# Kernel tuning notes

Measured on AMD Instinct MI355X. Metric: run time of the kernel, lower is better.

## Reference

```python
import jax, jax.numpy as jnp
import numpy as np

N_NODES = 50000


def gcn_layer(x, src, dst, W, b):
    # GCNConv: out = D^{-1/2} (A + I) D^{-1/2} (x W) + b
    n = x.shape[0]
    h = x @ W  # [N, C_out]
    # degree including self-loop (count of incoming edges at dst + 1)
    deg = jnp.zeros((n,), dtype=x.dtype).at[dst].add(1.0) + 1.0
    dinv_sqrt = jax.lax.rsqrt(deg)
    norm = dinv_sqrt[src] * dinv_sqrt[dst]  # [E]
    agg = jax.ops.segment_sum(h[src] * norm[:, None], dst, num_segments=n)
    # self-loop contribution: norm_ii = 1/deg_i
    agg = agg + h * (dinv_sqrt * dinv_sqrt)[:, None]
    return agg + b


def setup_inputs() -> dict:
    key = jax.random.key(0)
    k1, k2, k3, k4, k5, k6 = jax.random.split(key, 6)
    in_c, hid_c, out_c = 128, 128, 64
    x = jax.random.normal(k1, (N_NODES, in_c), dtype=jnp.float32)
    edge_index = jax.random.randint(k2, (2, 600000), 0, N_NODES, dtype=jnp.int64)
    W1 = jax.random.normal(k3, (in_c, hid_c), dtype=jnp.float32) * (1.0 / np.sqrt(in_c))
    b1 = jnp.zeros((hid_c,), dtype=jnp.float32)
    W2 = jax.random.normal(k4, (hid_c, out_c), dtype=jnp.float32) * (1.0 / np.sqrt(hid_c))
    b2 = jnp.zeros((out_c,), dtype=jnp.float32)
    return {"x": x, "edge_index": edge_index, "W1": W1, "b1": b1, "W2": W2, "b2": b2}


def reference(x, edge_index, W1, b1, W2, b2):
    src, dst = edge_index[0], edge_index[1]
    h = gcn_layer(x, src, dst, W1, b1)
    h = jax.nn.relu(h)
    out = gcn_layer(h, src, dst, W2, b2)
    return out
```

## Files before the change

### kernel.cpp

```cpp
#include <hip/hip_runtime.h>

#define IN_C 128
#define HID_C 128
#define OUT_C 64
#define CAP 40

typedef unsigned int uint;
typedef unsigned short ushort;
typedef __attribute__((ext_vector_type(8))) short short8;
typedef __attribute__((ext_vector_type(4))) float f32x4;

__device__ __forceinline__ float bf2f(ushort u) {
    return __uint_as_float(((uint)u) << 16);
}
__device__ __forceinline__ float bfl(uint u) {
    return __uint_as_float(u << 16);
}
__device__ __forceinline__ float bfh(uint u) {
    return __uint_as_float(u & 0xffff0000u);
}
__device__ __forceinline__ ushort f2bf(float f) {
    uint u = __float_as_uint(f);
    return (ushort)((u + 0x7fffu + ((u >> 16) & 1u)) >> 16);
}


__global__ void prep0_kernel(int* __restrict__ cursor, int n,
                             const float* __restrict__ W1, ushort* __restrict__ w1h,
                             ushort* __restrict__ w1l, const float* __restrict__ W2,
                             ushort* __restrict__ w2h, ushort* __restrict__ w2l) {
    int idx = blockIdx.x * blockDim.x + threadIdx.x;
    if (idx < n) {
        cursor[idx] = 0;
    } else if (idx < n + 128 * 128) {
        int i1 = idx - n;
        int k = i1 >> 7, c = i1 & 127;
        float w = W1[i1];
        ushort h = f2bf(w);
        ushort l = f2bf(w - bf2f(h));
        w1h[c * 128 + k] = h;
        w1l[c * 128 + k] = l;
    } else if (idx < n + 128 * 128 + 128 * 64) {
        int i2 = idx - n - 128 * 128;
        int k = i2 >> 6, c = i2 & 63;
        float w = W2[i2];
        ushort h = f2bf(w);
        ushort l = f2bf(w - bf2f(h));
        w2h[c * 128 + k] = h;
        w2l[c * 128 + k] = l;
    }
}


#define LSTR 40

__global__ __launch_bounds__(256) void gemm1_edge_kernel(
    const float* __restrict__ A, const ushort* __restrict__ BTh,
    const ushort* __restrict__ BTl, ushort* __restrict__ C, int M, int gblocks,
    const int* __restrict__ src, const int* __restrict__ dst,
    int* __restrict__ cursor, int* __restrict__ csr_src, int E) {
    constexpr int BN = 128;
    constexpr int NT = BN / 16;
    __shared__ ushort sAh[64 * LSTR], sAl[64 * LSTR];
    __shared__ ushort sBh[BN * LSTR], sBl[BN * LSTR];

    const int tid = threadIdx.x;

    if (blockIdx.x >= gblocks) {
        int e = (blockIdx.x - gblocks) * 256 + tid;
        if (e < E) {
            unsigned s = (unsigned)src[e];
            unsigned d = (unsigned)dst[e];
            if (s < (unsigned)M && d < (unsigned)M) {
                int p = atomicAdd(&cursor[d], 1);
                if (p < CAP) csr_src[d * CAP + p] = (int)s;
            }
        }
        return;
    }

    const int w = tid >> 6;
    const int lane = tid & 63;
    const int m = lane & 15;
    const int quad = lane >> 4;
    const int r0 = blockIdx.x * 64;

    f32x4 acc[NT];
#pragma unroll
    for (int t = 0; t < NT; ++t) acc[t] = (f32x4){0.f, 0.f, 0.f, 0.f};

    for (int k0 = 0; k0 < 128; k0 += 32) {
#pragma unroll
        for (int it = 0; it < 2; ++it) {
            int idx = tid + it * 256;
            int row = idx >> 3;
            int c4 = idx & 7;
            int grow = r0 + row;
            float4 v = make_float4(0.f, 0.f, 0.f, 0.f);
            if (grow < M) v = *(const float4*)&A[(size_t)grow * 128 + k0 + c4 * 4];
            ushort h0 = f2bf(v.x), h1 = f2bf(v.y), h2 = f2bf(v.z), h3 = f2bf(v.w);
            ushort l0 = f2bf(v.x - bf2f(h0)), l1 = f2bf(v.y - bf2f(h1));
            ushort l2 = f2bf(v.z - bf2f(h2)), l3 = f2bf(v.w - bf2f(h3));
            *(ushort4*)&sAh[row * LSTR + c4 * 4] = make_ushort4(h0, h1, h2, h3);
            *(ushort4*)&sAl[row * LSTR + c4 * 4] = make_ushort4(l0, l1, l2, l3);
        }
        for (int idx = tid; idx < BN * 4; idx += 256) {
            int row = idx >> 2;
            int c = idx & 3;
            *(uint4*)&sBh[row * LSTR + c * 8] = *(const uint4*)&BTh[row * 128 + k0 + c * 8];
            *(uint4*)&sBl[row * LSTR + c * 8] = *(const uint4*)&BTl[row * 128 + k0 + c * 8];
        }
        __syncthreads();

        short8 ah = *(const short8*)&sAh[(w * 16 + m) * LSTR + quad * 8];
        short8 al = *(const short8*)&sAl[(w * 16 + m) * LSTR + quad * 8];
#pragma unroll
        for (int t = 0; t < NT; ++t) {
            short8 bh = *(const short8*)&sBh[(t * 16 + m) * LSTR + quad * 8];
            short8 bl = *(const short8*)&sBl[(t * 16 + m) * LSTR + quad * 8];
            acc[t] = __builtin_amdgcn_mfma_f32_16x16x32_bf16(ah, bh, acc[t], 0, 0, 0);
            acc[t] = __builtin_amdgcn_mfma_f32_16x16x32_bf16(al, bh, acc[t], 0, 0, 0);
            acc[t] = __builtin_amdgcn_mfma_f32_16x16x32_bf16(ah, bl, acc[t], 0, 0, 0);
        }
        __syncthreads();
    }

#pragma unroll
    for (int t = 0; t < NT; ++t) {
#pragma unroll
        for (int r = 0; r < 4; ++r) {
            int row = r0 + w * 16 + quad * 4 + r;
            if (row < M) C[(size_t)row * BN + t * 16 + m] = f2bf(acc[t][r]);
        }
    }
}


template <int BN>
__global__ __launch_bounds__(256) void gemm_mfma_bf16A(const ushort* __restrict__ A,
                                                       const ushort* __restrict__ BTh,
                                                       const ushort* __restrict__ BTl,
                                                       ushort* __restrict__ C, int M) {
    constexpr int NT = BN / 16;
    __shared__ ushort sA[64 * LSTR];
    __shared__ ushort sBh[BN * LSTR], sBl[BN * LSTR];

    const int tid = threadIdx.x;
    const int w = tid >> 6;
    const int lane = tid & 63;
    const int m = lane & 15;
    const int quad = lane >> 4;
    const int r0 = blockIdx.x * 64;

    f32x4 acc[NT];
#pragma unroll
    for (int t = 0; t < NT; ++t) acc[t] = (f32x4){0.f, 0.f, 0.f, 0.f};

    for (int k0 = 0; k0 < 128; k0 += 32) {
        {
            int row = tid >> 2;
            int c = tid & 3;
            int grow = r0 + row;
            uint4 v = make_uint4(0, 0, 0, 0);
            if (grow < M) v = *(const uint4*)&A[(size_t)grow * 128 + k0 + c * 8];
            *(uint4*)&sA[row * LSTR + c * 8] = v;
        }
        for (int idx = tid; idx < BN * 4; idx += 256) {
            int row = idx >> 2;
            int c = idx & 3;
            *(uint4*)&sBh[row * LSTR + c * 8] = *(const uint4*)&BTh[row * 128 + k0 + c * 8];
            *(uint4*)&sBl[row * LSTR + c * 8] = *(const uint4*)&BTl[row * 128 + k0 + c * 8];
        }
        __syncthreads();

        short8 ah = *(const short8*)&sA[(w * 16 + m) * LSTR + quad * 8];
#pragma unroll
        for (int t = 0; t < NT; ++t) {
            short8 bh = *(const short8*)&sBh[(t * 16 + m) * LSTR + quad * 8];
            short8 bl = *(const short8*)&sBl[(t * 16 + m) * LSTR + quad * 8];
            acc[t] = __builtin_amdgcn_mfma_f32_16x16x32_bf16(ah, bh, acc[t], 0, 0, 0);
            acc[t] = __builtin_amdgcn_mfma_f32_16x16x32_bf16(ah, bl, acc[t], 0, 0, 0);
        }
        __syncthreads();
    }

#pragma unroll
    for (int t = 0; t < NT; ++t) {
#pragma unroll
        for (int r = 0; r < 4; ++r) {
            int row = r0 + w * 16 + quad * 4 + r;
            if (row < M) C[(size_t)row * 64 + t * 16 + m] = f2bf(acc[t][r]);
        }
    }
}


#define ACC8(v, nn)                                     \
    {                                                   \
        a0 += (nn) * bfl((v).x); a1 += (nn) * bfh((v).x); \
        a2 += (nn) * bfl((v).y); a3 += (nn) * bfh((v).y); \
        a4 += (nn) * bfl((v).z); a5 += (nn) * bfh((v).z); \
        a6 += (nn) * bfl((v).w); a7 += (nn) * bfh((v).w); \
    }

__global__ __launch_bounds__(256) void agg128_kernel(
    const uint4* __restrict__ hx, const int* __restrict__ csr_src,
    const int* __restrict__ degs, const float* __restrict__ bias,
    uint4* __restrict__ out, int n) {
    int node = blockIdx.x * 4 + (threadIdx.x >> 6);
    if (node >= n) return;
    int lane = threadIdx.x & 63;
    int quarter = lane >> 4;
    int q = lane & 15;
    int cnt = min(degs[node], CAP);
    float degf = (float)(cnt + 1);
    float dinv_d = rsqrtf(degf);
    int start = node * CAP;
    float a0 = 0.f, a1 = 0.f, a2 = 0.f, a3 = 0.f;
    float a4 = 0.f, a5 = 0.f, a6 = 0.f, a7 = 0.f;

    if (cnt > 0) {
        int es = (lane < cnt) ? csr_src[start + lane] : 0;
        int cs = (lane < cnt) ? degs[es] : 0;
        float en = rsqrtf((float)(cs + 1)) * dinv_d;
        int j = 0;
        for (; j + 8 <= cnt; j += 8) {
            int sA = __shfl(es, j + quarter);
            float nA = __shfl(en, j + quarter);
            int sB = __shfl(es, j + 4 + quarter);
            float nB = __shfl(en, j + 4 + quarter);
            uint4 vA = hx[(size_t)sA * 16 + q];
            uint4 vB = hx[(size_t)sB * 16 + q];
            ACC8(vA, nA);
            ACC8(vB, nB);
        }
        if (j < cnt) {
            int k0 = j + quarter;
            int s0 = __shfl(es, k0);
            float n0 = __shfl(en, k0);
            n0 = (k0 < cnt) ? n0 : 0.f;
            uint4 v0 = hx[(size_t)s0 * 16 + q];
            ACC8(v0, n0);
            if (j + 4 < cnt) {
                int k1 = j + 4 + quarter;
                int s1 = __shfl(es, k1);
                float n1 = __shfl(en, k1);
                n1 = (k1 < cnt) ? n1 : 0.f;
                uint4 v1 = hx[(size_t)s1 * 16 + q];
                ACC8(v1, n1);
            }
        }
    }

#pragma unroll
    for (int d = 16; d <= 32; d <<= 1) {
        a0 += __shfl_xor(a0, d); a1 += __shfl_xor(a1, d);
        a2 += __shfl_xor(a2, d); a3 += __shfl_xor(a3, d);
        a4 += __shfl_xor(a4, d); a5 += __shfl_xor(a5, d);
        a6 += __shfl_xor(a6, d); a7 += __shfl_xor(a7, d);
    }
    if (quarter == 0) {
        uint4 sv = hx[(size_t)node * 16 + q];
        float sn = 1.0f / degf;
        const float4* b4 = (const float4*)bias;
        float4 bA = b4[2 * q], bB = b4[2 * q + 1];
        float o0 = fmaxf(a0 + bfl(sv.x) * sn + bA.x, 0.f);
        float o1 = fmaxf(a1 + bfh(sv.x) * sn + bA.y, 0.f);
        float o2 = fmaxf(a2 + bfl(sv.y) * sn + bA.z, 0.f);
        float o3 = fmaxf(a3 + bfh(sv.y) * sn + bA.w, 0.f);
        float o4 = fmaxf(a4 + bfl(sv.z) * sn + bB.x, 0.f);
        float o5 = fmaxf(a5 + bfh(sv.z) * sn + bB.y, 0.f);
        float o6 = fmaxf(a6 + bfl(sv.w) * sn + bB.z, 0.f);
        float o7 = fmaxf(a7 + bfh(sv.w) * sn + bB.w, 0.f);
        uint4 u;
        u.x = (uint)f2bf(o0) | ((uint)f2bf(o1) << 16);
        u.y = (uint)f2bf(o2) | ((uint)f2bf(o3) << 16);
        u.z = (uint)f2bf(o4) | ((uint)f2bf(o5) << 16);
        u.w = (uint)f2bf(o6) | ((uint)f2bf(o7) << 16);
        out[(size_t)node * 16 + q] = u;
    }
}


__global__ __launch_bounds__(256) void agg64_kernel(
    const uint4* __restrict__ hx, const int* __restrict__ csr_src,
    const int* __restrict__ degs, const float* __restrict__ bias,
    float* __restrict__ out, int n) {
    int node = blockIdx.x * 4 + (threadIdx.x >> 6);
    if (node >= n) return;
    int lane = threadIdx.x & 63;
    int oct = lane >> 3;
    int q = lane & 7;
    int cnt = min(degs[node], CAP);
    float degf = (float)(cnt + 1);
    float dinv_d = rsqrtf(degf);
    int start = node * CAP;
    float a0 = 0.f, a1 = 0.f, a2 = 0.f, a3 = 0.f;
    float a4 = 0.f, a5 = 0.f, a6 = 0.f, a7 = 0.f;

    if (cnt > 0) {
        int es = (lane < cnt) ? csr_src[start + lane] : 0;
        int cs = (lane < cnt) ? degs[es] : 0;
        float en = rsqrtf((float)(cs + 1)) * dinv_d;
        int j = 0;
        for (; j + 16 <= cnt; j += 16) {
            int sA = __shfl(es, j + oct);
            float nA = __shfl(en, j + oct);
            int sB = __shfl(es, j + 8 + oct);
            float nB = __shfl(en, j + 8 + oct);
            uint4 vA = hx[(size_t)sA * 8 + q];
            uint4 vB = hx[(size_t)sB * 8 + q];
            ACC8(vA, nA);
            ACC8(vB, nB);
        }
        if (j < cnt) {
            int k0 = j + oct;
            int s0 = __shfl(es, k0);
            float n0 = __shfl(en, k0);
            n0 = (k0 < cnt) ? n0 : 0.f;
            uint4 v0 = hx[(size_t)s0 * 8 + q];
            ACC8(v0, n0);
            if (j + 8 < cnt) {
                int k1 = j + 8 + oct;
                int s1 = __shfl(es, k1);
                float n1 = __shfl(en, k1);
                n1 = (k1 < cnt) ? n1 : 0.f;
                uint4 v1 = hx[(size_t)s1 * 8 + q];
                ACC8(v1, n1);
            }
        }
    }

#pragma unroll
    for (int d = 8; d <= 32; d <<= 1) {
        a0 += __shfl_xor(a0, d); a1 += __shfl_xor(a1, d);
        a2 += __shfl_xor(a2, d); a3 += __shfl_xor(a3, d);
        a4 += __shfl_xor(a4, d); a5 += __shfl_xor(a5, d);
        a6 += __shfl_xor(a6, d); a7 += __shfl_xor(a7, d);
    }
    if (oct == 0) {
        uint4 sv = hx[(size_t)node * 8 + q];
        float sn = 1.0f / degf;
        const float4* b4 = (const float4*)bias;
        float4 bA = b4[2 * q], bB = b4[2 * q + 1];
        float4 oA, oB;
        oA.x = a0 + bfl(sv.x) * sn + bA.x;
        oA.y = a1 + bfh(sv.x) * sn + bA.y;
        oA.z = a2 + bfl(sv.y) * sn + bA.z;
        oA.w = a3 + bfh(sv.y) * sn + bA.w;
        oB.x = a4 + bfl(sv.z) * sn + bB.x;
        oB.y = a5 + bfh(sv.z) * sn + bB.y;
        oB.z = a6 + bfl(sv.w) * sn + bB.z;
        oB.w = a7 + bfh(sv.w) * sn + bB.w;
        float4* o4 = (float4*)out;
        o4[(size_t)node * 16 + 2 * q] = oA;
        o4[(size_t)node * 16 + 2 * q + 1] = oB;
    }
}


extern "C" void kernel_launch(void* const* d_in, const int* in_sizes, int n_in,
                              void* d_out, int out_size, void* d_ws, size_t ws_size,
                              hipStream_t stream) {
    (void)n_in; (void)out_size; (void)ws_size;
    const float* x  = (const float*)d_in[0];
    const int*   ei = (const int*)d_in[1];
    const float* W1 = (const float*)d_in[2];
    const float* b1 = (const float*)d_in[3];
    const float* W2 = (const float*)d_in[4];
    const float* b2 = (const float*)d_in[5];
    float* out = (float*)d_out;

    const int n = in_sizes[0] / IN_C;
    const int E = in_sizes[1] / 2;
    const int* src = ei;
    const int* dst = ei + E;

    char* ws = (char*)d_ws;
    size_t off = 0;
    auto alloc = [&](size_t bytes) -> void* {
        void* p = ws + off;
        off += (bytes + 1023) & ~(size_t)1023;
        return p;
    };

    ushort* w1h     = (ushort*)alloc(128 * 128 * 2);
    ushort* w1l     = (ushort*)alloc(128 * 128 * 2);
    ushort* w2h     = (ushort*)alloc(64 * 128 * 2);
    ushort* w2l     = (ushort*)alloc(64 * 128 * 2);
    int*    cursor  = (int*)   alloc((size_t)n * 4);
    int*    csr_src = (int*)   alloc((size_t)n * CAP * 4);
    ushort* h       = (ushort*)alloc((size_t)n * HID_C * 2);
    ushort* out1b   = (ushort*)alloc((size_t)n * HID_C * 2);

    const int gblocks = (n + 63) / 64;
    const int EB = (E + 255) / 256;
    const int ablocks = (n + 3) / 4;

    prep0_kernel<<<(n + 128 * 128 + 128 * 64 + 255) / 256, 256, 0, stream>>>(
        cursor, n, W1, w1h, w1l, W2, w2h, w2l);
    gemm1_edge_kernel<<<gblocks + EB, 256, 0, stream>>>(x, w1h, w1l, h, n, gblocks,
                                                        src, dst, cursor, csr_src, E);
    agg128_kernel<<<ablocks, 256, 0, stream>>>((const uint4*)h, csr_src, cursor,
                                               b1, (uint4*)out1b, n);
    gemm_mfma_bf16A<OUT_C><<<gblocks, 256, 0, stream>>>(out1b, w2h, w2l, h, n);
    agg64_kernel<<<ablocks, 256, 0, stream>>>((const uint4*)h, csr_src, cursor,
                                              b2, out, n);
}
```

Before: 175.1 us.

## Fuse layer-1 aggregation with layer-2 GEMM through shared memory

Replaces the separate agg128 and second GEMM kernels with one kernel. Each block aggregates 64 nodes, one wave handling 16 nodes in sequence, and writes the ReLU'd bf16 rows into LDS. It then runs the MFMA GEMM against W2 directly from LDS. This removes the global write and re-read of the intermediate activation and one launch. The cost is far fewer blocks in flight (one per 64 nodes instead of one per 4), so the latency-bound gather gets less parallelism.

```diff
diff --git a/kernel.cpp b/kernel.cpp
--- a/kernel.cpp
+++ b/kernel.cpp
@@ -4,6 +4,7 @@
 #define HID_C 128
 #define OUT_C 64
 #define CAP 40
+#define LSTR 40
 
 typedef unsigned int uint;
 typedef unsigned short ushort;
@@ -52,8 +53,6 @@
 }
 
 
-#define LSTR 40
-
 __global__ __launch_bounds__(256) void gemm1_edge_kernel(
     const float* __restrict__ A, const ushort* __restrict__ BTh,
     const ushort* __restrict__ BTl, ushort* __restrict__ C, int M, int gblocks,
@@ -136,65 +135,6 @@
 }
 
 
-template <int BN>
-__global__ __launch_bounds__(256) void gemm_mfma_bf16A(const ushort* __restrict__ A,
-                                                       const ushort* __restrict__ BTh,
-                                                       const ushort* __restrict__ BTl,
-                                                       ushort* __restrict__ C, int M) {
-    constexpr int NT = BN / 16;
-    __shared__ ushort sA[64 * LSTR];
-    __shared__ ushort sBh[BN * LSTR], sBl[BN * LSTR];
-
-    const int tid = threadIdx.x;
-    const int w = tid >> 6;
-    const int lane = tid & 63;
-    const int m = lane & 15;
-    const int quad = lane >> 4;
-    const int r0 = blockIdx.x * 64;
-
-    f32x4 acc[NT];
-#pragma unroll
-    for (int t = 0; t < NT; ++t) acc[t] = (f32x4){0.f, 0.f, 0.f, 0.f};
-
-    for (int k0 = 0; k0 < 128; k0 += 32) {
-        {
-            int row = tid >> 2;
-            int c = tid & 3;
-            int grow = r0 + row;
-            uint4 v = make_uint4(0, 0, 0, 0);
-            if (grow < M) v = *(const uint4*)&A[(size_t)grow * 128 + k0 + c * 8];
-            *(uint4*)&sA[row * LSTR + c * 8] = v;
-        }
-        for (int idx = tid; idx < BN * 4; idx += 256) {
-            int row = idx >> 2;
-            int c = idx & 3;
-            *(uint4*)&sBh[row * LSTR + c * 8] = *(const uint4*)&BTh[row * 128 + k0 + c * 8];
-            *(uint4*)&sBl[row * LSTR + c * 8] = *(const uint4*)&BTl[row * 128 + k0 + c * 8];
-        }
-        __syncthreads();
-
-        short8 ah = *(const short8*)&sA[(w * 16 + m) * LSTR + quad * 8];
-#pragma unroll
-        for (int t = 0; t < NT; ++t) {
-            short8 bh = *(const short8*)&sBh[(t * 16 + m) * LSTR + quad * 8];
-            short8 bl = *(const short8*)&sBl[(t * 16 + m) * LSTR + quad * 8];
-            acc[t] = __builtin_amdgcn_mfma_f32_16x16x32_bf16(ah, bh, acc[t], 0, 0, 0);
-            acc[t] = __builtin_amdgcn_mfma_f32_16x16x32_bf16(ah, bl, acc[t], 0, 0, 0);
-        }
-        __syncthreads();
-    }
-
-#pragma unroll
-    for (int t = 0; t < NT; ++t) {
-#pragma unroll
-        for (int r = 0; r < 4; ++r) {
-            int row = r0 + w * 16 + quad * 4 + r;
-            if (row < M) C[(size_t)row * 64 + t * 16 + m] = f2bf(acc[t][r]);
-        }
-    }
-}
-
-
 #define ACC8(v, nn)                                     \
     {                                                   \
         a0 += (nn) * bfl((v).x); a1 += (nn) * bfh((v).x); \
@@ -203,81 +143,129 @@
         a6 += (nn) * bfl((v).w); a7 += (nn) * bfh((v).w); \
     }
 
-__global__ __launch_bounds__(256) void agg128_kernel(
+
+__global__ __launch_bounds__(256) void agg_gemm2_kernel(
     const uint4* __restrict__ hx, const int* __restrict__ csr_src,
     const int* __restrict__ degs, const float* __restrict__ bias,
-    uint4* __restrict__ out, int n) {
-    int node = blockIdx.x * 4 + (threadIdx.x >> 6);
-    if (node >= n) return;
-    int lane = threadIdx.x & 63;
-    int quarter = lane >> 4;
-    int q = lane & 15;
-    int cnt = min(degs[node], CAP);
-    float degf = (float)(cnt + 1);
-    float dinv_d = rsqrtf(degf);
-    int start = node * CAP;
-    float a0 = 0.f, a1 = 0.f, a2 = 0.f, a3 = 0.f;
-    float a4 = 0.f, a5 = 0.f, a6 = 0.f, a7 = 0.f;
-
-    if (cnt > 0) {
-        int es = (lane < cnt) ? csr_src[start + lane] : 0;
-        int cs = (lane < cnt) ? degs[es] : 0;
-        float en = rsqrtf((float)(cs + 1)) * dinv_d;
-        int j = 0;
-        for (; j + 8 <= cnt; j += 8) {
-            int sA = __shfl(es, j + quarter);
-            float nA = __shfl(en, j + quarter);
-            int sB = __shfl(es, j + 4 + quarter);
-            float nB = __shfl(en, j + 4 + quarter);
-            uint4 vA = hx[(size_t)sA * 16 + q];
-            uint4 vB = hx[(size_t)sB * 16 + q];
-            ACC8(vA, nA);
-            ACC8(vB, nB);
-        }
-        if (j < cnt) {
-            int k0 = j + quarter;
-            int s0 = __shfl(es, k0);
-            float n0 = __shfl(en, k0);
-            n0 = (k0 < cnt) ? n0 : 0.f;
-            uint4 v0 = hx[(size_t)s0 * 16 + q];
-            ACC8(v0, n0);
-            if (j + 4 < cnt) {
-                int k1 = j + 4 + quarter;
-                int s1 = __shfl(es, k1);
-                float n1 = __shfl(en, k1);
-                n1 = (k1 < cnt) ? n1 : 0.f;
-                uint4 v1 = hx[(size_t)s1 * 16 + q];
-                ACC8(v1, n1);
-            }
-        }
-    }
-
-#pragma unroll
-    for (int d = 16; d <= 32; d <<= 1) {
-        a0 += __shfl_xor(a0, d); a1 += __shfl_xor(a1, d);
-        a2 += __shfl_xor(a2, d); a3 += __shfl_xor(a3, d);
-        a4 += __shfl_xor(a4, d); a5 += __shfl_xor(a5, d);
-        a6 += __shfl_xor(a6, d); a7 += __shfl_xor(a7, d);
-    }
-    if (quarter == 0) {
-        uint4 sv = hx[(size_t)node * 16 + q];
-        float sn = 1.0f / degf;
-        const float4* b4 = (const float4*)bias;
-        float4 bA = b4[2 * q], bB = b4[2 * q + 1];
-        float o0 = fmaxf(a0 + bfl(sv.x) * sn + bA.x, 0.f);
-        float o1 = fmaxf(a1 + bfh(sv.x) * sn + bA.y, 0.f);
-        float o2 = fmaxf(a2 + bfl(sv.y) * sn + bA.z, 0.f);
-        float o3 = fmaxf(a3 + bfh(sv.y) * sn + bA.w, 0.f);
-        float o4 = fmaxf(a4 + bfl(sv.z) * sn + bB.x, 0.f);
-        float o5 = fmaxf(a5 + bfh(sv.z) * sn + bB.y, 0.f);
-        float o6 = fmaxf(a6 + bfl(sv.w) * sn + bB.z, 0.f);
-        float o7 = fmaxf(a7 + bfh(sv.w) * sn + bB.w, 0.f);
-        uint4 u;
-        u.x = (uint)f2bf(o0) | ((uint)f2bf(o1) << 16);
-        u.y = (uint)f2bf(o2) | ((uint)f2bf(o3) << 16);
-        u.z = (uint)f2bf(o4) | ((uint)f2bf(o5) << 16);
-        u.w = (uint)f2bf(o6) | ((uint)f2bf(o7) << 16);
-        out[(size_t)node * 16 + q] = u;
+    const ushort* __restrict__ BTh, const ushort* __restrict__ BTl,
+    ushort* __restrict__ C, int n) {
+    __shared__ ushort sAf[4][64][LSTR];
+    __shared__ ushort sBh[64 * LSTR], sBl[64 * LSTR];
+
+    const int tid = threadIdx.x;
+    const int w = tid >> 6;
+    const int lane = tid & 63;
+    const int quarter = lane >> 4;
+    const int q = lane & 15;
+    const int r0 = blockIdx.x * 64;
+
+    for (int i = 0; i < 16; ++i) {
+        const int lrow = w * 16 + i;
+        const int node = r0 + lrow;
+        uint4 u = make_uint4(0u, 0u, 0u, 0u);
+        if (node < n) {
+            int cnt = min(degs[node], CAP);
+            float degf = (float)(cnt + 1);
+            float dinv_d = rsqrtf(degf);
+            int start = node * CAP;
+            float a0 = 0.f, a1 = 0.f, a2 = 0.f, a3 = 0.f;
+            float a4 = 0.f, a5 = 0.f, a6 = 0.f, a7 = 0.f;
+
+            if (cnt > 0) {
+                int es = (lane < cnt) ? csr_src[start + lane] : 0;
+                int cs = (lane < cnt) ? degs[es] : 0;
+                float en = rsqrtf((float)(cs + 1)) * dinv_d;
+                int j = 0;
+                for (; j + 8 <= cnt; j += 8) {
+                    int sA = __shfl(es, j + quarter);
+                    float nA = __shfl(en, j + quarter);
+                    int sB = __shfl(es, j + 4 + quarter);
+                    float nB = __shfl(en, j + 4 + quarter);
+                    uint4 vA = hx[(size_t)sA * 16 + q];
+                    uint4 vB = hx[(size_t)sB * 16 + q];
+                    ACC8(vA, nA);
+                    ACC8(vB, nB);
+                }
+                if (j < cnt) {
+                    int k0 = j + quarter;
+                    int s0 = __shfl(es, k0);
+                    float n0 = __shfl(en, k0);
+                    n0 = (k0 < cnt) ? n0 : 0.f;
+                    uint4 v0 = hx[(size_t)s0 * 16 + q];
+                    ACC8(v0, n0);
+                    if (j + 4 < cnt) {
+                        int k1 = j + 4 + quarter;
+                        int s1 = __shfl(es, k1);
+                        float n1 = __shfl(en, k1);
+                        n1 = (k1 < cnt) ? n1 : 0.f;
+                        uint4 v1 = hx[(size_t)s1 * 16 + q];
+                        ACC8(v1, n1);
+                    }
+                }
+            }
+
+#pragma unroll
+            for (int d = 16; d <= 32; d <<= 1) {
+                a0 += __shfl_xor(a0, d); a1 += __shfl_xor(a1, d);
+                a2 += __shfl_xor(a2, d); a3 += __shfl_xor(a3, d);
+                a4 += __shfl_xor(a4, d); a5 += __shfl_xor(a5, d);
+                a6 += __shfl_xor(a6, d); a7 += __shfl_xor(a7, d);
+            }
+            if (quarter == 0) {
+                uint4 sv = hx[(size_t)node * 16 + q];
+                float sn = 1.0f / degf;
+                const float4* b4 = (const float4*)bias;
+                float4 bA = b4[2 * q], bB = b4[2 * q + 1];
+                float o0 = fmaxf(a0 + bfl(sv.x) * sn + bA.x, 0.f);
+                float o1 = fmaxf(a1 + bfh(sv.x) * sn + bA.y, 0.f);
+                float o2 = fmaxf(a2 + bfl(sv.y) * sn + bA.z, 0.f);
+                float o3 = fmaxf(a3 + bfh(sv.y) * sn + bA.w, 0.f);
+                float o4 = fmaxf(a4 + bfl(sv.z) * sn + bB.x, 0.f);
+                float o5 = fmaxf(a5 + bfh(sv.z) * sn + bB.y, 0.f);
+                float o6 = fmaxf(a6 + bfl(sv.w) * sn + bB.z, 0.f);
+                float o7 = fmaxf(a7 + bfh(sv.w) * sn + bB.w, 0.f);
+                u.x = (uint)f2bf(o0) | ((uint)f2bf(o1) << 16);
+                u.y = (uint)f2bf(o2) | ((uint)f2bf(o3) << 16);
+                u.z = (uint)f2bf(o4) | ((uint)f2bf(o5) << 16);
+                u.w = (uint)f2bf(o6) | ((uint)f2bf(o7) << 16);
+            }
+        }
+        if (quarter == 0) {
+            *(uint4*)&sAf[q >> 2][lrow][(q & 3) * 8] = u;
+        }
+    }
+
+    f32x4 acc[4];
+#pragma unroll
+    for (int t = 0; t < 4; ++t) acc[t] = (f32x4){0.f, 0.f, 0.f, 0.f};
+
+    for (int k0 = 0; k0 < 128; k0 += 32) {
+        {
+            int row = tid >> 2;
+            int c = tid & 3;
+            *(uint4*)&sBh[row * LSTR + c * 8] = *(const uint4*)&BTh[row * 128 + k0 + c * 8];
+            *(uint4*)&sBl[row * LSTR + c * 8] = *(const uint4*)&BTl[row * 128 + k0 + c * 8];
+        }
+        __syncthreads();
+
+        short8 ah = *(const short8*)&sAf[k0 >> 5][w * 16 + q][quarter * 8];
+#pragma unroll
+        for (int t = 0; t < 4; ++t) {
+            short8 bh = *(const short8*)&sBh[(t * 16 + q) * LSTR + quarter * 8];
+            short8 bl = *(const short8*)&sBl[(t * 16 + q) * LSTR + quarter * 8];
+            acc[t] = __builtin_amdgcn_mfma_f32_16x16x32_bf16(ah, bh, acc[t], 0, 0, 0);
+            acc[t] = __builtin_amdgcn_mfma_f32_16x16x32_bf16(ah, bl, acc[t], 0, 0, 0);
+        }
+        __syncthreads();
+    }
+
+#pragma unroll
+    for (int t = 0; t < 4; ++t) {
+#pragma unroll
+        for (int r = 0; r < 4; ++r) {
+            int row = r0 + w * 16 + quarter * 4 + r;
+            if (row < n) C[(size_t)row * 64 + t * 16 + q] = f2bf(acc[t][r]);
+        }
     }
 }
 
@@ -390,8 +378,8 @@
     ushort* w2l     = (ushort*)alloc(64 * 128 * 2);
     int*    cursor  = (int*)   alloc((size_t)n * 4);
     int*    csr_src = (int*)   alloc((size_t)n * CAP * 4);
-    ushort* h       = (ushort*)alloc((size_t)n * HID_C * 2);
-    ushort* out1b   = (ushort*)alloc((size_t)n * HID_C * 2);
+    ushort* h1      = (ushort*)alloc((size_t)n * HID_C * 2);
+    ushort* h2      = (ushort*)alloc((size_t)n * HID_C * 2);
 
     const int gblocks = (n + 63) / 64;
     const int EB = (E + 255) / 256;
@@ -399,11 +387,10 @@
 
     prep0_kernel<<<(n + 128 * 128 + 128 * 64 + 255) / 256, 256, 0, stream>>>(
         cursor, n, W1, w1h, w1l, W2, w2h, w2l);
-    gemm1_edge_kernel<<<gblocks + EB, 256, 0, stream>>>(x, w1h, w1l, h, n, gblocks,
+    gemm1_edge_kernel<<<gblocks + EB, 256, 0, stream>>>(x, w1h, w1l, h1, n, gblocks,
                                                         src, dst, cursor, csr_src, E);
-    agg128_kernel<<<ablocks, 256, 0, stream>>>((const uint4*)h, csr_src, cursor,
-                                               b1, (uint4*)out1b, n);
-    gemm_mfma_bf16A<OUT_C><<<gblocks, 256, 0, stream>>>(out1b, w2h, w2l, h, n);
-    agg64_kernel<<<ablocks, 256, 0, stream>>>((const uint4*)h, csr_src, cursor,
+    agg_gemm2_kernel<<<gblocks, 256, 0, stream>>>((const uint4*)h1, csr_src, cursor,
+                                                  b1, w2h, w2l, h2, n);
+    agg64_kernel<<<ablocks, 256, 0, stream>>>((const uint4*)h2, csr_src, cursor,
                                               b2, out, n);
 }
```

New measurement: 187.8 us. +7.2%, slower.
